# Kernel tuning notes

Measured on AMD Instinct MI355X. Metric: run time of the kernel, lower is better.

The kernel has to match this reference:

```python
import jax, jax.numpy as jnp
import numpy as np

V = 50257      # output vocab size
EMB = 1024     # embedding_size
HD = 1024      # decoder_hidden_size
HE = 1024      # encoder_hidden_size
L = 128        # max_src_length
B = 64         # batch_size
SCALE = 0.02


def setup_inputs() -> dict:
    key = jax.random.key(0)
    ks = jax.random.split(key, 16)
    inp = {
        "input_tensor": jax.random.randint(ks[0], (1, B), 0, V),
        "hidden": jax.random.normal(ks[1], (1, B, HD), dtype=jnp.float32),
        "encoder_outputs": jax.random.normal(ks[2], (L, B, HE), dtype=jnp.float32),
        "batch_size": B,
        # parameters
        "emb_table": jax.random.normal(ks[3], (V, EMB), dtype=jnp.float32) * SCALE,
        "attn_w": jax.random.normal(ks[4], (L, EMB + HD), dtype=jnp.float32) * SCALE,
        "attn_b": jnp.zeros((L,), dtype=jnp.float32),
        "comb_w": jax.random.normal(ks[5], (HE, EMB + HE), dtype=jnp.float32) * SCALE,
        "comb_b": jnp.zeros((HE,), dtype=jnp.float32),
        "w_ih": jax.random.normal(ks[6], (3 * HD, HE), dtype=jnp.float32) * SCALE,
        "w_hh": jax.random.normal(ks[7], (3 * HD, HD), dtype=jnp.float32) * SCALE,
        "b_ih": jnp.zeros((3 * HD,), dtype=jnp.float32),
        "b_hh": jnp.zeros((3 * HD,), dtype=jnp.float32),
        "out_w": jax.random.normal(ks[8], (V, HD), dtype=jnp.float32) * SCALE,
        "out_b": jnp.zeros((V,), dtype=jnp.float32),
    }
    return inp


def reference(input_tensor, hidden, encoder_outputs, batch_size,
              emb_table, attn_w, attn_b, comb_w, comb_b,
              w_ih, w_hh, b_ih, b_hh, out_w, out_b):
    # Embedding lookup: [1,B] -> [B,EMB] (dropout is identity at eval)
    embedded = emb_table[input_tensor[0]]
    h0 = hidden[0]  # [B,HD]

    # Bahdanau-style attention over max_src_length positions
    attn_in = jnp.concatenate([embedded, h0], axis=1)            # [B, EMB+HD]
    attn_weights = jax.nn.softmax(attn_in @ attn_w.T + attn_b, axis=1)  # [B,L]

    # context = sum_l attn[b,l] * enc[l,b,:]  (equiv of permuted bmm)
    ctx = jnp.einsum('lbe,bl->be', encoder_outputs, attn_weights)  # [B,HE]

    # attn_combine + relu
    comb = jnp.concatenate([embedded, ctx], axis=1) @ comb_w.T + comb_b
    x = jax.nn.relu(comb)  # [B,HE]

    # single-step GRU (PyTorch gate layout: r, z, n)
    gi = x @ w_ih.T + b_ih     # [B,3*HD]
    gh = h0 @ w_hh.T + b_hh    # [B,3*HD]
    i_r, i_z, i_n = jnp.split(gi, 3, axis=1)
    h_r, h_z, h_n = jnp.split(gh, 3, axis=1)
    r = jax.nn.sigmoid(i_r + h_r)
    z = jax.nn.sigmoid(i_z + h_z)
    n = jnp.tanh(i_n + r * h_n)
    h_new = (1.0 - z) * n + z * h0  # [B,HD]

    # output projection + log_softmax
    output = jax.nn.log_softmax(h_new @ out_w.T + out_b, axis=1)  # [B,V]

    return output, h_new[None], attn_weights
```

## Files before the change

kernel.cpp:

```cpp
#include <hip/hip_runtime.h>
#include <math.h>

#define V 50257
#define B 64
#define HD 1024
#define LSRC 128
#define NBLK 786

typedef float v4f __attribute__((ext_vector_type(4)));
typedef __bf16 v8bf __attribute__((ext_vector_type(8)));
typedef unsigned short v8us __attribute__((ext_vector_type(8)));

__device__ inline unsigned short bf_rne(float x) {
    unsigned int u = __float_as_uint(x);
    return (unsigned short)((u + 0x7fffu + ((u >> 16) & 1u)) >> 16);
}
__device__ inline unsigned int pk2_rne(float x, float y) {
    return (unsigned int)bf_rne(x) | ((unsigned int)bf_rne(y) << 16);
}

__global__ void k_prep(const int* __restrict__ idx, const float* __restrict__ hidden,
                       const float* __restrict__ emb, unsigned short* __restrict__ catB,
                       unsigned short* __restrict__ actC) {
    int i = blockIdx.x * 256 + threadIdx.x;
    int b = i >> 11, k = i & 2047;
    unsigned short v;
    if (k < 1024) {
        v = bf_rne(emb[(size_t)idx[b] * 1024 + k]);
        actC[b * 2048 + k] = v;
    } else {
        v = bf_rne(hidden[b * 1024 + (k - 1024)]);
    }
    catB[b * 2048 + k] = v;
}

__device__ __forceinline__ void mm_core(const float* __restrict__ W,
                                        const unsigned short* __restrict__ act, int as_,
                                        float* __restrict__ P, int M, int K, int Kc,
                                        int mx, int ks, int tid) {
    int wave = tid >> 6, lane = tid & 63;
    int quad = lane >> 4, r16 = lane & 15;
    int row0 = mx * 64 + wave * 16;
    int kbase = ks * Kc;
    const float* wr = W + (size_t)(row0 + r16) * K + kbase + quad * 8;
    const unsigned short* ab = act + kbase + quad * 8;
    v4f acc[4] = {};
    for (int kk = 0; kk < Kc; kk += 32) {
        float4 p0 = *(const float4*)(wr + kk);
        float4 p1 = *(const float4*)(wr + kk + 4);
        union { unsigned int u[4]; v8us v; } A;
        A.u[0] = pk2_rne(p0.x, p0.y); A.u[1] = pk2_rne(p0.z, p0.w);
        A.u[2] = pk2_rne(p1.x, p1.y); A.u[3] = pk2_rne(p1.z, p1.w);
        v8bf af = __builtin_bit_cast(v8bf, A.v);
        #pragma unroll
        for (int nt = 0; nt < 4; ++nt) {
            v8us bu = *(const v8us*)(ab + (size_t)(nt * 16 + r16) * as_ + kk);
            v8bf bf = __builtin_bit_cast(v8bf, bu);
            acc[nt] = __builtin_amdgcn_mfma_f32_16x16x32_bf16(af, bf, acc[nt], 0, 0, 0);
        }
    }
    float* po = P + (size_t)ks * 64 * M;
    #pragma unroll
    for (int nt = 0; nt < 4; ++nt) {
        int b = nt * 16 + r16;
        float4 val = make_float4(acc[nt][0], acc[nt][1], acc[nt][2], acc[nt][3]);
        *(float4*)(po + (size_t)b * M + row0 + quad * 4) = val;
    }
}

__global__ __launch_bounds__(256) void k_mm(const float* __restrict__ W,
                                            const unsigned short* __restrict__ act,
                                            float* __restrict__ P, int M, int K, int Kc,
                                            int as_) {
    mm_core(W, act, as_, P, M, K, Kc, blockIdx.x, blockIdx.y, threadIdx.x);
}

__global__ __launch_bounds__(256) void k_mm2(const float* __restrict__ Wc,
                                             const unsigned short* __restrict__ actC,
                                             float* __restrict__ Pc,
                                             const float* __restrict__ Wh,
                                             const unsigned short* __restrict__ h0B,
                                             float* __restrict__ Ph) {
    int bx = blockIdx.x;
    if (bx < 16) mm_core(Wc, actC, 2048, Pc, 1024, 2048, 512, bx, blockIdx.y, threadIdx.x);
    else         mm_core(Wh, h0B, 2048, Ph, 3072, 1024, 256, bx - 16, blockIdx.y, threadIdx.x);
}

__global__ void k_ctxs(const float* __restrict__ Pa, const float* __restrict__ attn_b,
                       const float* __restrict__ enc, unsigned short* __restrict__ actC,
                       float* __restrict__ out2) {
    __shared__ float a_sh[128];
    __shared__ float red[8];
    int b = blockIdx.y, tid = threadIdx.x;
    int lane = tid & 63, wave = tid >> 6;
    float x = -1e30f;
    if (tid < 128) {
        x = attn_b[tid];
        #pragma unroll
        for (int ks = 0; ks < 4; ++ks) x += Pa[(ks * 64 + b) * 128 + tid];
    }
    float m = x;
    #pragma unroll
    for (int off = 32; off; off >>= 1) m = fmaxf(m, __shfl_xor(m, off));
    if (lane == 0) red[wave] = m;
    __syncthreads();
    m = fmaxf(fmaxf(red[0], red[1]), fmaxf(red[2], red[3]));
    float e = (tid < 128) ? __expf(x - m) : 0.f;
    float ssum = e;
    #pragma unroll
    for (int off = 32; off; off >>= 1) ssum += __shfl_xor(ssum, off);
    if (lane == 0) red[4 + wave] = ssum;
    __syncthreads();
    float stot = red[4] + red[5] + red[6] + red[7];
    if (tid < 128) {
        float w = e / stot;
        a_sh[tid] = w;
        if (blockIdx.x == 0) out2[b * 128 + tid] = w;
    }
    __syncthreads();
    int e0 = blockIdx.x * 256 + tid;
    float acc0 = 0.f, acc1 = 0.f;
    #pragma unroll 8
    for (int l = 0; l < 128; l += 2) {
        acc0 += a_sh[l]     * enc[((size_t)(l * 64) + b) * 1024 + e0];
        acc1 += a_sh[l + 1] * enc[((size_t)((l + 1) * 64) + b) * 1024 + e0];
    }
    actC[b * 2048 + 1024 + e0] = bf_rne(acc0 + acc1);
}

__global__ void k_redc(const float* __restrict__ Pc, const float* __restrict__ comb_b,
                       unsigned short* __restrict__ xB) {
    int i = blockIdx.x * 256 + threadIdx.x;
    int b = i >> 10, k = i & 1023;
    float s = comb_b[k];
    #pragma unroll
    for (int ss = 0; ss < 4; ++ss) s += Pc[((size_t)ss * 64 + b) * 1024 + k];
    s = fmaxf(s, 0.f);
    xB[b * 1024 + k] = bf_rne(s);
}

__global__ void k_gates(const float* __restrict__ Pi, const float* __restrict__ Ph,
                        const float* __restrict__ b_ih, const float* __restrict__ b_hh,
                        const float* __restrict__ hidden, float* __restrict__ out1,
                        unsigned short* __restrict__ hbf) {
    int i = blockIdx.x * 256 + threadIdx.x;
    int b = i >> 10, u = i & 1023;
    float ir = b_ih[u], iz = b_ih[1024 + u], in_ = b_ih[2048 + u];
    float hr = b_hh[u], hz = b_hh[1024 + u], hn = b_hh[2048 + u];
    #pragma unroll
    for (int s = 0; s < 4; ++s) {
        const float* pi = Pi + ((size_t)s * 64 + b) * 3072;
        const float* ph = Ph + ((size_t)s * 64 + b) * 3072;
        ir += pi[u]; iz += pi[1024 + u]; in_ += pi[2048 + u];
        hr += ph[u]; hz += ph[1024 + u]; hn += ph[2048 + u];
    }
    float r = 1.f / (1.f + __expf(-(ir + hr)));
    float z = 1.f / (1.f + __expf(-(iz + hz)));
    float n = tanhf(in_ + r * hn);
    float h0 = hidden[b * 1024 + u];
    float h = (1.f - z) * n + z * h0;
    out1[b * 1024 + u] = h;
    hbf[b * 1024 + u] = bf_rne(h);
}

__global__ __launch_bounds__(256) void k_gemm(const float* __restrict__ Wt,
                                              const unsigned short* __restrict__ hbf,
                                              const float* __restrict__ out_b,
                                              float* __restrict__ out0,
                                              float* __restrict__ m_part,
                                              float* __restrict__ s_part) {
    __shared__ float sm[4][64], ss[4][64];
    int tid = threadIdx.x;
    int wave = tid >> 6, lane = tid & 63;
    int quad = lane >> 4, r16 = lane & 15;
    int v0 = blockIdx.x * 64 + wave * 16;
    int va = min(v0 + r16, V - 1);
    const float* wr = Wt + (size_t)va * 1024 + quad * 8;
    const unsigned short* ab = hbf + quad * 8;
    v4f acc[4] = {};
    for (int kk = 0; kk < 1024; kk += 32) {
        float4 p0 = *(const float4*)(wr + kk);
        float4 p1 = *(const float4*)(wr + kk + 4);
        union { unsigned int u[4]; v8us v; } A;
        A.u[0] = pk2_rne(p0.x, p0.y); A.u[1] = pk2_rne(p0.z, p0.w);
        A.u[2] = pk2_rne(p1.x, p1.y); A.u[3] = pk2_rne(p1.z, p1.w);
        v8bf af = __builtin_bit_cast(v8bf, A.v);
        #pragma unroll
        for (int nt = 0; nt < 4; ++nt) {
            v8us bu = *(const v8us*)(ab + (size_t)(nt * 16 + r16) * 1024 + kk);
            v8bf bf = __builtin_bit_cast(v8bf, bu);
            acc[nt] = __builtin_amdgcn_mfma_f32_16x16x32_bf16(af, bf, acc[nt], 0, 0, 0);
        }
    }
    #pragma unroll
    for (int nt = 0; nt < 4; ++nt) {
        int b = nt * 16 + r16;
        float lm = -1e30f, lsum = 0.f;
        #pragma unroll
        for (int r = 0; r < 4; ++r) {
            int v = v0 + quad * 4 + r;
            if (v < V) {
                float x = acc[nt][r] + out_b[v];
                out0[(size_t)b * V + v] = x;
                float nm = fmaxf(lm, x);
                lsum = lsum * __expf(lm - nm) + __expf(x - nm);
                lm = nm;
            }
        }
        #pragma unroll
        for (int off = 16; off <= 32; off <<= 1) {
            float om = __shfl_xor(lm, off), os = __shfl_xor(lsum, off);
            float nm = fmaxf(lm, om);
            lsum = lsum * __expf(lm - nm) + os * __expf(om - nm);
            lm = nm;
        }
        if (quad == 0) { sm[wave][b] = lm; ss[wave][b] = lsum; }
    }
    __syncthreads();
    if (tid < 64) {
        float M2 = sm[0][tid], S2 = ss[0][tid];
        #pragma unroll
        for (int w = 1; w < 4; ++w) {
            float nm = fmaxf(M2, sm[w][tid]);
            S2 = S2 * __expf(M2 - nm) + ss[w][tid] * __expf(sm[w][tid] - nm);
            M2 = nm;
        }
        m_part[(size_t)tid * NBLK + blockIdx.x] = M2;
        s_part[(size_t)tid * NBLK + blockIdx.x] = S2;
    }
}

__global__ void k_comb(const float* __restrict__ m_part, const float* __restrict__ s_part,
                       float* __restrict__ lse) {
    __shared__ float sm[4], ss[4];
    int b = blockIdx.x, tid = threadIdx.x;
    int lane = tid & 63, wave = tid >> 6;
    float m = -1e30f, s = 0.f;
    for (int i = tid; i < NBLK; i += 256) {
        float om = m_part[(size_t)b * NBLK + i], os = s_part[(size_t)b * NBLK + i];
        float nm = fmaxf(m, om);
        s = s * __expf(m - nm) + os * __expf(om - nm);
        m = nm;
    }
    #pragma unroll
    for (int off = 32; off; off >>= 1) {
        float om = __shfl_xor(m, off), os = __shfl_xor(s, off);
        float nm = fmaxf(m, om);
        s = s * __expf(m - nm) + os * __expf(om - nm);
        m = nm;
    }
    if (lane == 0) { sm[wave] = m; ss[wave] = s; }
    __syncthreads();
    if (tid == 0) {
        float M = sm[0], S = ss[0];
        #pragma unroll
        for (int w = 1; w < 4; ++w) {
            float nm = fmaxf(M, sm[w]);
            S = S * __expf(M - nm) + ss[w] * __expf(sm[w] - nm);
            M = nm;
        }
        lse[b] = M + __logf(S);
    }
}

__global__ void k_final(float* __restrict__ out0, const float* __restrict__ lse) {
    int b = blockIdx.y;
    float l = lse[b];
    int base = blockIdx.x * 2048 + threadIdx.x;
    #pragma unroll
    for (int j = 0; j < 8; ++j) {
        int v = base + j * 256;
        if (v < V) out0[(size_t)b * V + v] -= l;
    }
}

extern "C" void kernel_launch(void* const* d_in, const int* in_sizes, int n_in,
                              void* d_out, int out_size, void* d_ws, size_t ws_size,
                              hipStream_t stream) {
    const int*   input_tensor = (const int*)d_in[0];
    const float* hidden  = (const float*)d_in[1];
    const float* enc     = (const float*)d_in[2];
    const float* emb     = (const float*)d_in[4];
    const float* attn_w  = (const float*)d_in[5];
    const float* attn_b  = (const float*)d_in[6];
    const float* comb_w  = (const float*)d_in[7];
    const float* comb_b  = (const float*)d_in[8];
    const float* w_ih    = (const float*)d_in[9];
    const float* w_hh    = (const float*)d_in[10];
    const float* b_ih    = (const float*)d_in[11];
    const float* b_hh    = (const float*)d_in[12];
    const float* out_w   = (const float*)d_in[13];
    const float* out_b   = (const float*)d_in[14];

    float* out0 = (float*)d_out;
    float* out1 = out0 + (size_t)B * V;
    float* out2 = out1 + B * HD;

    float* ws = (float*)d_ws;
    float* Pa     = ws;
    float* Pc     = ws + 32768;
    float* lse    = ws + 294912;
    float* m_part = ws + 294976;
    float* s_part = ws + 345280;
    unsigned short* catB = (unsigned short*)(ws + 395584);
    unsigned short* actC = (unsigned short*)(ws + 461120);
    unsigned short* xB   = (unsigned short*)(ws + 526656);
    unsigned short* hbf  = (unsigned short*)(ws + 543040);

    float* Pi = out0;
    float* Ph = out0 + 4 * 64 * 3072;

    k_prep<<<512, 256, 0, stream>>>(input_tensor, hidden, emb, catB, actC);
    k_mm<<<dim3(2, 4), 256, 0, stream>>>(attn_w, catB, Pa, 128, 2048, 512, 2048);
    k_ctxs<<<dim3(4, 64), 256, 0, stream>>>(Pa, attn_b, enc, actC, out2);
    k_mm2<<<dim3(64, 4), 256, 0, stream>>>(comb_w, actC, Pc, w_hh, catB + 1024, Ph);
    k_redc<<<256, 256, 0, stream>>>(Pc, comb_b, xB);
    k_mm<<<dim3(48, 4), 256, 0, stream>>>(w_ih, xB, Pi, 3072, 1024, 256, 1024);
    k_gates<<<256, 256, 0, stream>>>(Pi, Ph, b_ih, b_hh, hidden, out1, hbf);
    k_gemm<<<NBLK, 256, 0, stream>>>(out_w, hbf, out_b, out0, m_part, s_part);
    k_comb<<<64, 256, 0, stream>>>(m_part, s_part, lse);
    k_final<<<dim3(25, 64), 256, 0, stream>>>(out0, lse);
}
```

Baseline: 541.3 us.

## Stage output weight tiles through double-buffered LDS and drop block-level softmax reduction

```diff
diff --git a/kernel.cpp b/kernel.cpp
--- a/kernel.cpp
+++ b/kernel.cpp
@@ -6,6 +6,7 @@
 #define HD 1024
 #define LSRC 128
 #define NBLK 786
+#define NP (NBLK * 4)
 
 typedef float v4f __attribute__((ext_vector_type(4)));
 typedef __bf16 v8bf __attribute__((ext_vector_type(8)));
@@ -119,13 +120,15 @@
     }
     __syncthreads();
     int e0 = blockIdx.x * 256 + tid;
-    float acc0 = 0.f, acc1 = 0.f;
-    #pragma unroll 8
-    for (int l = 0; l < 128; l += 2) {
-        acc0 += a_sh[l]     * enc[((size_t)(l * 64) + b) * 1024 + e0];
+    float acc0 = 0.f, acc1 = 0.f, acc2 = 0.f, acc3 = 0.f;
+    #pragma unroll
+    for (int l = 0; l < 128; l += 4) {
+        acc0 += a_sh[l]     * enc[((size_t)((l + 0) * 64) + b) * 1024 + e0];
         acc1 += a_sh[l + 1] * enc[((size_t)((l + 1) * 64) + b) * 1024 + e0];
-    }
-    actC[b * 2048 + 1024 + e0] = bf_rne(acc0 + acc1);
+        acc2 += a_sh[l + 2] * enc[((size_t)((l + 2) * 64) + b) * 1024 + e0];
+        acc3 += a_sh[l + 3] * enc[((size_t)((l + 3) * 64) + b) * 1024 + e0];
+    }
+    actC[b * 2048 + 1024 + e0] = bf_rne((acc0 + acc1) + (acc2 + acc3));
 }
 
 __global__ void k_redc(const float* __restrict__ Pc, const float* __restrict__ comb_b,
@@ -163,35 +166,65 @@
     hbf[b * 1024 + u] = bf_rne(h);
 }
 
-__global__ __launch_bounds__(256) void k_gemm(const float* __restrict__ Wt,
-                                              const unsigned short* __restrict__ hbf,
-                                              const float* __restrict__ out_b,
-                                              float* __restrict__ out0,
-                                              float* __restrict__ m_part,
-                                              float* __restrict__ s_part) {
-    __shared__ float sm[4][64], ss[4][64];
+__global__ __launch_bounds__(256, 2) void k_gemm(const float* __restrict__ Wt,
+                                                 const unsigned short* __restrict__ hbf,
+                                                 const float* __restrict__ out_b,
+                                                 float* __restrict__ out0,
+                                                 float* __restrict__ m_part,
+                                                 float* __restrict__ s_part) {
+    __shared__ float Abuf[2][64 * 128];
     int tid = threadIdx.x;
     int wave = tid >> 6, lane = tid & 63;
     int quad = lane >> 4, r16 = lane & 15;
-    int v0 = blockIdx.x * 64 + wave * 16;
-    int va = min(v0 + r16, V - 1);
-    const float* wr = Wt + (size_t)va * 1024 + quad * 8;
-    const unsigned short* ab = hbf + quad * 8;
+    int row0 = blockIdx.x * 64;
+    int v0 = row0 + wave * 16;
+
+    int srow = tid >> 2;
+    int scol = (tid & 3) * 32;
+    int grow = min(row0 + srow, V - 1);
+    const float* gsrc = Wt + (size_t)grow * 1024 + scol;
+    float* lflat = &Abuf[0][0];
+
+    float4 st[8];
+    #pragma unroll
+    for (int j = 0; j < 8; ++j) st[j] = *(const float4*)(gsrc + j * 4);
+    #pragma unroll
+    for (int j = 0; j < 8; ++j) *(float4*)(lflat + tid * 32 + j * 4) = st[j];
+    __syncthreads();
+
+    const unsigned short* bq = hbf + (size_t)r16 * 1024 + quad * 8;
     v4f acc[4] = {};
-    for (int kk = 0; kk < 1024; kk += 32) {
-        float4 p0 = *(const float4*)(wr + kk);
-        float4 p1 = *(const float4*)(wr + kk + 4);
-        union { unsigned int u[4]; v8us v; } A;
-        A.u[0] = pk2_rne(p0.x, p0.y); A.u[1] = pk2_rne(p0.z, p0.w);
-        A.u[2] = pk2_rne(p1.x, p1.y); A.u[3] = pk2_rne(p1.z, p1.w);
-        v8bf af = __builtin_bit_cast(v8bf, A.v);
-        #pragma unroll
-        for (int nt = 0; nt < 4; ++nt) {
-            v8us bu = *(const v8us*)(ab + (size_t)(nt * 16 + r16) * 1024 + kk);
-            v8bf bf = __builtin_bit_cast(v8bf, bu);
-            acc[nt] = __builtin_amdgcn_mfma_f32_16x16x32_bf16(af, bf, acc[nt], 0, 0, 0);
-        }
-    }
+    for (int t = 0; t < 8; ++t) {
+        if (t + 1 < 8) {
+            const float* gs = gsrc + (t + 1) * 128;
+            #pragma unroll
+            for (int j = 0; j < 8; ++j) st[j] = *(const float4*)(gs + j * 4);
+        }
+        const float* ar = &Abuf[t & 1][(wave * 16 + r16) * 128 + quad * 8];
+        #pragma unroll
+        for (int kk = 0; kk < 128; kk += 32) {
+            float4 p0 = *(const float4*)(ar + kk);
+            float4 p1 = *(const float4*)(ar + kk + 4);
+            union { unsigned int u[4]; v8us v; } A;
+            A.u[0] = pk2_rne(p0.x, p0.y); A.u[1] = pk2_rne(p0.z, p0.w);
+            A.u[2] = pk2_rne(p1.x, p1.y); A.u[3] = pk2_rne(p1.z, p1.w);
+            v8bf af = __builtin_bit_cast(v8bf, A.v);
+            int ko = t * 128 + kk;
+            #pragma unroll
+            for (int nt = 0; nt < 4; ++nt) {
+                v8us bu = *(const v8us*)(bq + nt * 16384 + ko);
+                v8bf bf = __builtin_bit_cast(v8bf, bu);
+                acc[nt] = __builtin_amdgcn_mfma_f32_16x16x32_bf16(af, bf, acc[nt], 0, 0, 0);
+            }
+        }
+        if (t + 1 < 8) {
+            float* lf = &Abuf[(t + 1) & 1][0];
+            #pragma unroll
+            for (int j = 0; j < 8; ++j) *(float4*)(lf + tid * 32 + j * 4) = st[j];
+        }
+        __syncthreads();
+    }
+
     #pragma unroll
     for (int nt = 0; nt < 4; ++nt) {
         int b = nt * 16 + r16;
@@ -214,19 +247,10 @@
             lsum = lsum * __expf(lm - nm) + os * __expf(om - nm);
             lm = nm;
         }
-        if (quad == 0) { sm[wave][b] = lm; ss[wave][b] = lsum; }
-    }
-    __syncthreads();
-    if (tid < 64) {
-        float M2 = sm[0][tid], S2 = ss[0][tid];
-        #pragma unroll
-        for (int w = 1; w < 4; ++w) {
-            float nm = fmaxf(M2, sm[w][tid]);
-            S2 = S2 * __expf(M2 - nm) + ss[w][tid] * __expf(sm[w][tid] - nm);
-            M2 = nm;
-        }
-        m_part[(size_t)tid * NBLK + blockIdx.x] = M2;
-        s_part[(size_t)tid * NBLK + blockIdx.x] = S2;
+        if (quad == 0) {
+            m_part[(size_t)b * NP + blockIdx.x * 4 + wave] = lm;
+            s_part[(size_t)b * NP + blockIdx.x * 4 + wave] = lsum;
+        }
     }
 }
 
@@ -236,8 +260,8 @@
     int b = blockIdx.x, tid = threadIdx.x;
     int lane = tid & 63, wave = tid >> 6;
     float m = -1e30f, s = 0.f;
-    for (int i = tid; i < NBLK; i += 256) {
-        float om = m_part[(size_t)b * NBLK + i], os = s_part[(size_t)b * NBLK + i];
+    for (int i = tid; i < NP; i += 256) {
+        float om = m_part[(size_t)b * NP + i], os = s_part[(size_t)b * NP + i];
         float nm = fmaxf(m, om);
         s = s * __expf(m - nm) + os * __expf(om - nm);
         m = nm;
@@ -301,11 +325,11 @@
     float* Pc     = ws + 32768;
     float* lse    = ws + 294912;
     float* m_part = ws + 294976;
-    float* s_part = ws + 345280;
-    unsigned short* catB = (unsigned short*)(ws + 395584);
-    unsigned short* actC = (unsigned short*)(ws + 461120);
-    unsigned short* xB   = (unsigned short*)(ws + 526656);
-    unsigned short* hbf  = (unsigned short*)(ws + 543040);
+    float* s_part = ws + 496192;
+    unsigned short* catB = (unsigned short*)(ws + 697408);
+    unsigned short* actC = (unsigned short*)(ws + 762944);
+    unsigned short* xB   = (unsigned short*)(ws + 828480);
+    unsigned short* hbf  = (unsigned short*)(ws + 844864);
 
     float* Pi = out0;
     float* Ph = out0 + 4 * 64 * 3072;
```

After: 553.7 us. 1.02x slower.
